# Kernel tuning notes

Measured on AMD Instinct MI355X. Metric: run time of the kernel, lower is better.

Reference implementation:

```python
import jax, jax.numpy as jnp
import numpy as np

TOPK = 13
ALPHA = 1.0
BETA = 6.0
EPS = 1e-9


def _make_boxes(key, lead_shape, img=640.0):
    kc, ks = jax.random.split(key)
    c = jax.random.uniform(kc, lead_shape + (2,), minval=0.0, maxval=img)
    s = jax.random.uniform(ks, lead_shape + (2,), minval=16.0, maxval=160.0)
    return jnp.concatenate([c - s * 0.5, c + s * 0.5], axis=-1)


def setup_inputs() -> dict:
    key = jax.random.key(0)
    ks = jax.random.split(key, 8)
    B, L, C, N, K = 32, 8400, 1, 64, 17
    pred_scores = jax.random.uniform(ks[0], (B, L, C), dtype=jnp.float32)
    pred_bboxes = _make_boxes(ks[1], (B, L))
    pred_poses = jax.random.normal(ks[2], (B, L, K, 3), dtype=jnp.float32)
    anchor_points = jax.random.uniform(ks[3], (L, 2), minval=0.0, maxval=640.0)
    gt_labels = jax.random.randint(ks[4], (B, N, 1), 0, C)
    gt_bboxes = _make_boxes(ks[5], (B, N))
    gt_poses = jax.random.normal(ks[6], (B, N, K, 3), dtype=jnp.float32)
    counts = jax.random.randint(ks[7], (B,), 8, N + 1)
    pad_gt_mask = (jnp.arange(N)[None, :] < counts[:, None]).astype(jnp.float32)[..., None]
    return dict(pred_scores=pred_scores, pred_bboxes=pred_bboxes, pred_poses=pred_poses,
                anchor_points=anchor_points, gt_labels=gt_labels, gt_bboxes=gt_bboxes,
                gt_poses=gt_poses, pad_gt_mask=pad_gt_mask, bg_index=C)


def _batch_iou(box1, box2, eps=EPS):
    # box1: [B,n,4], box2: [B,L,4] -> [B,n,L]
    a = box1[:, :, None, :]
    b = box2[:, None, :, :]
    lt = jnp.maximum(a[..., :2], b[..., :2])
    rb = jnp.minimum(a[..., 2:], b[..., 2:])
    wh = jnp.clip(rb - lt, 0.0)
    inter = wh[..., 0] * wh[..., 1]
    area_a = (a[..., 2] - a[..., 0]) * (a[..., 3] - a[..., 1])
    area_b = (b[..., 2] - b[..., 0]) * (b[..., 3] - b[..., 1])
    return inter / (area_a + area_b - inter + eps)


def _points_in_boxes(points, bboxes, eps=EPS):
    # points: [L,2], bboxes: [B,n,4] -> [B,n,L] float
    x, y = points[:, 0], points[:, 1]
    x1 = bboxes[..., 0:1]; y1 = bboxes[..., 1:2]
    x2 = bboxes[..., 2:3]; y2 = bboxes[..., 3:4]
    m = jnp.minimum(jnp.minimum(x - x1, y - y1), jnp.minimum(x2 - x, y2 - y))
    return (m > eps).astype(bboxes.dtype)


def _gather_topk_anchors(metrics, topk, topk_mask):
    # metrics: [B,n,L]; topk_mask: [B,n,1]
    B, n, L = metrics.shape
    _, idxs = jax.lax.top_k(metrics, topk)  # [B,n,K]
    is_in_topk = jnp.zeros_like(metrics).at[
        jnp.arange(B)[:, None, None], jnp.arange(n)[None, :, None], idxs].add(1.0)
    return is_in_topk * topk_mask


def _compute_max_iou_anchor(ious):
    # ious: [B,n,L] -> one-hot over gt dim of argmax gt per anchor
    n = ious.shape[-2]
    idx = jnp.argmax(ious, axis=-2)  # [B,L]
    return (jnp.arange(n)[None, :, None] == idx[:, None, :]).astype(ious.dtype)


def reference(pred_scores, pred_bboxes, pred_poses, anchor_points, gt_labels,
              gt_bboxes, gt_poses, pad_gt_mask, bg_index):
    B, L, C = pred_scores.shape
    n = gt_bboxes.shape[1]
    K = pred_poses.shape[2]

    ious = _batch_iou(gt_bboxes, pred_bboxes)  # [B,n,L]
    scores_t = jnp.transpose(pred_scores, (0, 2, 1))  # [B,C,L]
    bbox_cls_scores = scores_t[jnp.arange(B)[:, None], gt_labels[..., 0]]  # [B,n,L]
    alignment_metrics = (bbox_cls_scores ** ALPHA) * (ious ** BETA)

    is_in_gts = _points_in_boxes(anchor_points, gt_bboxes)  # [B,n,L]
    is_in_topk = _gather_topk_anchors(alignment_metrics * is_in_gts, TOPK, pad_gt_mask)
    mask_positive = is_in_topk * is_in_gts * pad_gt_mask  # [B,n,L]
    mask_positive_sum = mask_positive.sum(axis=-2)  # [B,L]

    # resolve anchors assigned to multiple gts by max IoU (no-op when no conflicts)
    mask_multiple_gts = jnp.broadcast_to((mask_positive_sum[:, None, :] > 1), mask_positive.shape)
    is_max_iou = _compute_max_iou_anchor(ious)
    mask_positive = jnp.where(mask_multiple_gts, is_max_iou, mask_positive)
    mask_positive_sum = mask_positive.sum(axis=-2)

    assigned_gt_index = jnp.argmax(mask_positive, axis=-2)  # [B,L]
    assigned_gt_index = assigned_gt_index + jnp.arange(B)[:, None] * n  # flat offset
    flat = assigned_gt_index.reshape(-1)

    assigned_labels = jnp.take(gt_labels.reshape(-1), flat).reshape(B, L)
    assigned_labels = jnp.where(mask_positive_sum > 0, assigned_labels,
                                jnp.full_like(assigned_labels, bg_index))
    assigned_bboxes = gt_bboxes.reshape(-1, 4)[flat].reshape(B, L, 4)
    assigned_poses = gt_poses.reshape(-1, K, 3)[flat].reshape(B, L, K, 3)

    one_hot = jax.nn.one_hot(assigned_labels, C + 1, dtype=pred_scores.dtype)
    keep = np.array([i for i in range(C + 1) if i != bg_index])
    assigned_scores = one_hot[..., keep]  # [B,L,C]

    am = alignment_metrics * mask_positive
    max_metrics = am.max(axis=-1, keepdims=True)  # [B,n,1]
    max_ious = (ious * mask_positive).max(axis=-1, keepdims=True)
    am = am / (max_metrics + EPS) * max_ious
    am = am.max(axis=-2)[..., None]  # [B,L,1]
    assigned_scores = assigned_scores * am

    return assigned_labels, assigned_bboxes, assigned_poses, assigned_scores, assigned_gt_index
```

## Files before the change

kernel.cpp:

```cpp
#include <hip/hip_runtime.h>
#include <hip/hip_bf16.h>

#define BB    32
#define LL    8400
#define NGT   64
#define CCH   1
#define KPT   17
#define NTOPK 13
#define POOL  2048
#define NBIN  32

#define OFF_LAB  ((size_t)0)
#define OFF_BOX  ((size_t)268800)
#define OFF_POSE ((size_t)1344000)
#define OFF_SC   ((size_t)15052800)
#define OFF_GI   ((size_t)15321600)


__device__ __forceinline__ float iou_pair(float gx1, float gy1, float gx2, float gy2,
                                          float px1, float py1, float px2, float py2)
{
#pragma clang fp contract(off)
    float ltx = fmaxf(gx1, px1);
    float lty = fmaxf(gy1, py1);
    float rbx = fminf(gx2, px2);
    float rby = fminf(gy2, py2);
    float w = fmaxf(rbx - ltx, 0.0f);
    float h = fmaxf(rby - lty, 0.0f);
    float inter = w * h;
    float ag = (gx2 - gx1) * (gy2 - gy1);
    float ap = (px2 - px1) * (py2 - py1);
    return inter / (ag + ap - inter + 1e-9f);
}

__device__ __forceinline__ bool in_box(float ax, float ay,
                                       float gx1, float gy1, float gx2, float gy2)
{
#pragma clang fp contract(off)
    float m = fminf(fminf(ax - gx1, ay - gy1), fminf(gx2 - ax, gy2 - ay));
    return m > 1e-9f;
}

__device__ __forceinline__ float pow6(float x)
{
#pragma clang fp contract(off)
    float x2 = x * x;
    return (x2 * x2) * x2;
}

__device__ __forceinline__ int bin_of(float x)
{
    int v = (int)floorf(x * 0.05f);
    return v < 0 ? 0 : (v > NBIN - 1 ? NBIN - 1 : v);
}


__global__ __launch_bounds__(256) void clear_kernel(float4* __restrict__ p, int n4)
{
    int t = blockIdx.x * 256 + threadIdx.x;
    if (t < n4) p[t] = make_float4(0.f, 0.f, 0.f, 0.f);
}


__global__ __launch_bounds__(1024) void build_bins_kernel(
    const float* __restrict__ anchor_points,
    int*   __restrict__ bin_start,
    int*   __restrict__ bin_id,
    float2* __restrict__ bin_xy)
{
    __shared__ int c[NBIN * NBIN];
    __shared__ int off[NBIN * NBIN];
    int tid = threadIdx.x;

    c[tid] = 0;
    __syncthreads();
    for (int l = tid; l < LL; l += 1024) {
        float2 ap = reinterpret_cast<const float2*>(anchor_points)[l];
        int bin = bin_of(ap.y) * NBIN + bin_of(ap.x);
        atomicAdd(&c[bin], 1);
    }
    __syncthreads();

    off[tid] = c[tid];
    __syncthreads();
    for (int s = 1; s < NBIN * NBIN; s <<= 1) {
        int v = (tid >= s) ? off[tid - s] : 0;
        __syncthreads();
        off[tid] += v;
        __syncthreads();
    }
    bin_start[tid + 1] = off[tid];
    if (tid == 0) bin_start[0] = 0;
    c[tid] = 0;
    __syncthreads();

    for (int l = tid; l < LL; l += 1024) {
        float2 ap = reinterpret_cast<const float2*>(anchor_points)[l];
        int bin = bin_of(ap.y) * NBIN + bin_of(ap.x);
        int st = (bin == 0) ? 0 : off[bin - 1];
        int slot = st + atomicAdd(&c[bin], 1);
        bin_id[slot] = l;
        bin_xy[slot] = ap;
    }
}


__global__ __launch_bounds__(256) void topk_kernel(
    const float* __restrict__ pred_scores,
    const float* __restrict__ pred_bboxes,
    const float* __restrict__ anchor_points,
    const int*   __restrict__ gt_labels,
    const float* __restrict__ gt_bboxes,
    const float* __restrict__ pad_gt_mask,
    const int*   __restrict__ bin_start,
    const int*   __restrict__ bin_id,
    const float2* __restrict__ bin_xy,
    unsigned*    __restrict__ cells)
{
    __shared__ unsigned long long pool[POOL];
    __shared__ unsigned long long wlists[4 * NTOPK];
    __shared__ int cnt;

    int b = blockIdx.x >> 6;
    int i = blockIdx.x & 63;
    if (pad_gt_mask[b * NGT + i] == 0.0f) return;

    int tid = threadIdx.x;
    if (tid == 0) cnt = 0;
    __syncthreads();

    int gbase = (b * NGT + i) * 4;
    float gx1 = gt_bboxes[gbase + 0];
    float gy1 = gt_bboxes[gbase + 1];
    float gx2 = gt_bboxes[gbase + 2];
    float gy2 = gt_bboxes[gbase + 3];
    int lbl = gt_labels[b * NGT + i];

    int lane = tid & 63;
    int wave = tid >> 6;

    if (tid < 2 * NTOPK) {
        float2 ap = reinterpret_cast<const float2*>(anchor_points)[tid];
        if (!in_box(ap.x, ap.y, gx1, gy1, gx2, gy2)) {
            int slot = atomicAdd(&cnt, 1);
            pool[slot] = (unsigned long long)(0xFFFFFFFFu - (unsigned)tid);
        }
    }

    int bx0 = bin_of(gx1), bx1 = bin_of(gx2);
    int by0 = bin_of(gy1), by1 = bin_of(gy2);
    for (int by = by0; by <= by1; ++by) {
        int s = bin_start[by * NBIN + bx0];
        int e = bin_start[by * NBIN + bx1 + 1];
        for (int t = s + tid; t < e; t += 256) {
            float2 ap = bin_xy[t];
            if (in_box(ap.x, ap.y, gx1, gy1, gx2, gy2)) {
                int l = bin_id[t];
                int pidx = b * LL + l;
                float4 pb = reinterpret_cast<const float4*>(pred_bboxes)[pidx];
                float iou = iou_pair(gx1, gy1, gx2, gy2, pb.x, pb.y, pb.z, pb.w);
                float score = pred_scores[pidx * CCH + lbl];
                float v = score * pow6(iou);
                int slot = atomicAdd(&cnt, 1);
                if (slot < POOL) {
                    pool[slot] =
                        ((unsigned long long)__float_as_uint(v) << 32) |
                        (unsigned long long)(0xFFFFFFFFu - (unsigned)l);
                }
            }
        }
    }
    __syncthreads();

    int total = cnt;
    if (total <= POOL) {
#pragma unroll
        for (int k = 0; k < NTOPK; ++k) {
            unsigned long long lm = 0;
            int li = -1;
            for (int e = wave * 64 + lane; e < total; e += 256) {
                unsigned long long pv = pool[e];
                if (pv > lm) { lm = pv; li = e; }
            }
            unsigned long long m = lm;
#pragma unroll
            for (int off = 32; off > 0; off >>= 1) {
                unsigned long long o = __shfl_xor(m, off);
                m = o > m ? o : m;
            }
            if (lane == 0) wlists[wave * NTOPK + k] = m;
            if (li >= 0 && lm == m) pool[li] = 0;
        }
    } else {
        unsigned long long prev = ~0ull;
        for (int k = 0; k < NTOPK; ++k) {
            unsigned long long lm = 0;
            for (int l = wave * 64 + lane; l < LL; l += 256) {
                int pidx = b * LL + l;
                float4 pb = reinterpret_cast<const float4*>(pred_bboxes)[pidx];
                float iou = iou_pair(gx1, gy1, gx2, gy2, pb.x, pb.y, pb.z, pb.w);
                float score = pred_scores[pidx * CCH + lbl];
                float metric = score * pow6(iou);
                float2 ap = reinterpret_cast<const float2*>(anchor_points)[l];
                float v = in_box(ap.x, ap.y, gx1, gy1, gx2, gy2) ? metric : 0.0f;
                unsigned long long key =
                    ((unsigned long long)__float_as_uint(v) << 32) |
                    (unsigned long long)(0xFFFFFFFFu - (unsigned)l);
                if (key < prev && key > lm) lm = key;
            }
            unsigned long long m = lm;
#pragma unroll
            for (int off = 32; off > 0; off >>= 1) {
                unsigned long long o = __shfl_xor(m, off);
                m = o > m ? o : m;
            }
            if (lane == 0) wlists[wave * NTOPK + k] = m;
            prev = m;
        }
    }
    __syncthreads();

    if (tid == 0) {
        int p0 = 0, p1 = 0, p2 = 0, p3 = 0;
        for (int k = 0; k < NTOPK; ++k) {
            unsigned long long k0 = wlists[0 * NTOPK + p0];
            unsigned long long k1 = wlists[1 * NTOPK + p1];
            unsigned long long k2 = wlists[2 * NTOPK + p2];
            unsigned long long k3 = wlists[3 * NTOPK + p3];
            unsigned long long m01 = k0 >= k1 ? k0 : k1;
            unsigned long long m23 = k2 >= k3 ? k2 : k3;
            unsigned long long m = m01 >= m23 ? m01 : m23;
            if (m == k0)      ++p0;
            else if (m == k1) ++p1;
            else if (m == k2) ++p2;
            else              ++p3;
            if (m == 0ull) continue;

            unsigned lw = 0xFFFFFFFFu - (unsigned)(m & 0xFFFFFFFFull);
            float v = __uint_as_float((unsigned)(m >> 32));
            bool posw;
            if (v > 0.0f) {
                posw = true;
            } else {
                float2 ap = reinterpret_cast<const float2*>(anchor_points)[lw];
                posw = in_box(ap.x, ap.y, gx1, gy1, gx2, gy2);
            }
            if (posw)
                atomicAdd(&cells[b * LL + lw], 1u + ((unsigned)i << 8));
        }
    }
}


__global__ __launch_bounds__(256) void decode_kernel(
    const float* __restrict__ pred_scores,
    const float* __restrict__ pred_bboxes,
    const int*   __restrict__ gt_labels,
    const float* __restrict__ gt_bboxes,
    const unsigned* __restrict__ cells,
    int*      __restrict__ assigned,
    unsigned* __restrict__ rowmax_metric,
    unsigned* __restrict__ rowmax_iou)
{
    __shared__ float gsh[NGT * 4];
    int b = blockIdx.y;
    int tid = threadIdx.x;
    for (int k = tid; k < NGT * 4; k += 256) gsh[k] = gt_bboxes[b * NGT * 4 + k];
    __syncthreads();

    int l = blockIdx.x * 256 + tid;
    if (l >= LL) return;
    int idx = b * LL + l;

    unsigned cell = cells[idx];
    int cnt = (int)(cell & 0xFFu);
    if (cnt == 0) { assigned[idx] = -1; return; }

    float px1 = pred_bboxes[idx * 4 + 0];
    float py1 = pred_bboxes[idx * 4 + 1];
    float px2 = pred_bboxes[idx * 4 + 2];
    float py2 = pred_bboxes[idx * 4 + 3];

    int istar;
    if (cnt == 1) {
        int v = (int)(cell >> 8);
        istar = (v >= 0 && v < NGT) ? v : 0;
    } else {
        float best = -1.0f;
        int bi = 0;
        for (int i = 0; i < NGT; ++i) {
            float iou = iou_pair(gsh[i * 4 + 0], gsh[i * 4 + 1], gsh[i * 4 + 2], gsh[i * 4 + 3],
                                 px1, py1, px2, py2);
            if (iou > best) { best = iou; bi = i; }
        }
        istar = bi;
    }
    assigned[idx] = istar;

    float iou = iou_pair(gsh[istar * 4 + 0], gsh[istar * 4 + 1], gsh[istar * 4 + 2], gsh[istar * 4 + 3],
                         px1, py1, px2, py2);
    int lbl = gt_labels[b * NGT + istar];
    float score = pred_scores[idx * CCH + lbl];
    float met = score * pow6(iou);
    atomicMax(&rowmax_metric[b * NGT + istar], __float_as_uint(met));
    atomicMax(&rowmax_iou[b * NGT + istar], __float_as_uint(iou));
}


__global__ __launch_bounds__(256) void write_kernel(
    const float* __restrict__ pred_scores,
    const float* __restrict__ pred_bboxes,
    const int*   __restrict__ gt_labels,
    const float* __restrict__ gt_bboxes,
    const int*      __restrict__ assigned,
    const unsigned* __restrict__ rowmax_metric,
    const unsigned* __restrict__ rowmax_iou,
    const int*   __restrict__ bg_ptr,
    float* __restrict__ out)
{
    __shared__ float gsh[NGT * 4];
    int b = blockIdx.y;
    int tid = threadIdx.x;
    for (int k = tid; k < NGT * 4; k += 256) gsh[k] = gt_bboxes[b * NGT * 4 + k];
    __syncthreads();

    int l = blockIdx.x * 256 + tid;
    if (l >= LL) return;
    int idx = b * LL + l;

    int a = assigned[idx];
    bool pos = a >= 0;
    int agi = pos ? a : 0;
    int bg = *bg_ptr;
    int lbl = pos ? gt_labels[b * NGT + agi] : bg;

    out[OFF_LAB + (size_t)idx] = (float)lbl;
    out[OFF_GI + (size_t)idx]  = (float)(b * NGT + agi);

    float4 box;
    box.x = gsh[agi * 4 + 0];
    box.y = gsh[agi * 4 + 1];
    box.z = gsh[agi * 4 + 2];
    box.w = gsh[agi * 4 + 3];
    reinterpret_cast<float4*>(out + OFF_BOX)[idx] = box;

    float am = 0.0f;
    if (pos) {
        float px1 = pred_bboxes[idx * 4 + 0];
        float py1 = pred_bboxes[idx * 4 + 1];
        float px2 = pred_bboxes[idx * 4 + 2];
        float py2 = pred_bboxes[idx * 4 + 3];
        float iou = iou_pair(box.x, box.y, box.z, box.w, px1, py1, px2, py2);
        float score = pred_scores[idx * CCH + gt_labels[b * NGT + a]];
        float met = score * pow6(iou);
        float mm = __uint_as_float(rowmax_metric[b * NGT + a]);
        float mi = __uint_as_float(rowmax_iou[b * NGT + a]);
        am = met / (mm + 1e-9f) * mi;
    }
    int kc = (bg == 0) ? 1 : 0;
    out[OFF_SC + (size_t)idx] = (lbl == kc) ? am : 0.0f;
}


__global__ __launch_bounds__(256) void pose_kernel(
    const float* __restrict__ gt_poses,
    const int*   __restrict__ assigned,
    float* __restrict__ out_poses)
{
    const int TOT4 = BB * LL * KPT * 3 / 4;
    int c = blockIdx.x * 256 + threadIdx.x;
    if (c >= TOT4) return;
    int e0 = c * 4;
    float r[4];
#pragma unroll
    for (int u = 0; u < 4; ++u) {
        int e = e0 + u;
        int anchor = e / (KPT * 3);
        int j = e - anchor * (KPT * 3);
        int b = anchor / LL;
        int a = assigned[anchor];
        int agi = a >= 0 ? a : 0;
        r[u] = gt_poses[(size_t)(b * NGT + agi) * (KPT * 3) + j];
    }
    float4 v;
    v.x = r[0]; v.y = r[1]; v.z = r[2]; v.w = r[3];
    reinterpret_cast<float4*>(out_poses)[c] = v;
}


extern "C" void kernel_launch(void* const* d_in, const int* in_sizes, int n_in,
                              void* d_out, int out_size, void* d_ws, size_t ws_size,
                              hipStream_t stream)
{
    const float* pred_scores   = (const float*)d_in[0];
    const float* pred_bboxes   = (const float*)d_in[1];
    const float* anchor_points = (const float*)d_in[3];
    const int*   gt_labels     = (const int*)d_in[4];
    const float* gt_bboxes     = (const float*)d_in[5];
    const float* gt_poses      = (const float*)d_in[6];
    const float* pad_gt_mask   = (const float*)d_in[7];
    const int*   bg_ptr        = (const int*)d_in[8];

    char* ws = (char*)d_ws;
    unsigned* cells         = (unsigned*)ws;
    unsigned* rowmax_metric = (unsigned*)(ws + 1075200);
    unsigned* rowmax_iou    = (unsigned*)(ws + 1083392);
    int*      assigned      = (int*)(ws + 1091584);
    int*      bin_start     = (int*)(ws + 2166784);
    int*      bin_id        = (int*)(ws + 2170888);
    float2*   bin_xy        = (float2*)(ws + 2204488);

    const int N4 = 1091584 / 16;
    clear_kernel<<<(N4 + 255) / 256, 256, 0, stream>>>((float4*)d_ws, N4);

    build_bins_kernel<<<1, 1024, 0, stream>>>(anchor_points, bin_start, bin_id, bin_xy);

    topk_kernel<<<BB * NGT, 256, 0, stream>>>(
        pred_scores, pred_bboxes, anchor_points, gt_labels, gt_bboxes, pad_gt_mask,
        bin_start, bin_id, bin_xy, cells);

    dim3 gridBL((LL + 255) / 256, BB);
    decode_kernel<<<gridBL, 256, 0, stream>>>(
        pred_scores, pred_bboxes, gt_labels, gt_bboxes, cells,
        assigned, rowmax_metric, rowmax_iou);

    write_kernel<<<gridBL, 256, 0, stream>>>(
        pred_scores, pred_bboxes, gt_labels, gt_bboxes,
        assigned, rowmax_metric, rowmax_iou, bg_ptr, (float*)d_out);

    const int TOT4 = BB * LL * KPT * 3 / 4;
    pose_kernel<<<(TOT4 + 255) / 256, 256, 0, stream>>>(
        gt_poses, assigned, (float*)d_out + OFF_POSE);
}
```

Baseline: 95.66 us.

## Parallelize anchor binning across blocks and shrink topk to one wave per GT

The single-block anchor binning kernel is split into three kernels: a parallel count with global atomics, a single-block scan, and a parallel scatter. The topk kernel now runs one 64-thread wave per GT, which drops the per-wave candidate lists and the serial 4-way merge on thread 0. Each of the first 13 lanes keeps one winner and issues its own atomic. The pool shrinks to 1024 entries to lower LDS use and raise occupancy. The risks are more frequent fallback to the full-scan path for large boxes, extra launch overhead, and less parallelism within each GT.

After: 88.64 us, median of 2. -7.3%, faster.

```diff
diff --git a/kernel.cpp b/kernel.cpp
--- a/kernel.cpp
+++ b/kernel.cpp
@@ -7,7 +7,7 @@
 #define CCH   1
 #define KPT   17
 #define NTOPK 13
-#define POOL  2048
+#define POOL  1024
 #define NBIN  32
 
 #define OFF_LAB  ((size_t)0)
@@ -15,6 +15,16 @@
 #define OFF_POSE ((size_t)1344000)
 #define OFF_SC   ((size_t)15052800)
 #define OFF_GI   ((size_t)15321600)
+
+#define WS_CELLS    0
+#define WS_RM       1075200
+#define WS_RI       1083392
+#define WS_ASSIGNED 1091584
+#define WS_BINCNT   2166784
+#define WS_BINSTART 2170880
+#define WS_BINCUR   2174984
+#define WS_BINID    2179080
+#define WS_BINXY    2212680
 
 
 __device__ __forceinline__ float iou_pair(float gx1, float gy1, float gx2, float gy2,
@@ -55,33 +65,34 @@
 }
 
 
-__global__ __launch_bounds__(256) void clear_kernel(float4* __restrict__ p, int n4)
-{
+__global__ __launch_bounds__(256) void clear_kernel(char* __restrict__ ws)
+{
+    const int N4A = 1091584 / 16;
+    const int N4B = 4096 / 16;
     int t = blockIdx.x * 256 + threadIdx.x;
-    if (t < n4) p[t] = make_float4(0.f, 0.f, 0.f, 0.f);
-}
-
-
-__global__ __launch_bounds__(1024) void build_bins_kernel(
-    const float* __restrict__ anchor_points,
-    int*   __restrict__ bin_start,
-    int*   __restrict__ bin_id,
-    float2* __restrict__ bin_xy)
-{
-    __shared__ int c[NBIN * NBIN];
+    if (t < N4A)
+        reinterpret_cast<float4*>(ws + WS_CELLS)[t] = make_float4(0.f, 0.f, 0.f, 0.f);
+    else if (t < N4A + N4B)
+        reinterpret_cast<float4*>(ws + WS_BINCNT)[t - N4A] = make_float4(0.f, 0.f, 0.f, 0.f);
+}
+
+
+__global__ __launch_bounds__(256) void count_kernel(
+    const float* __restrict__ anchor_points, int* __restrict__ bin_cnt)
+{
+    int l = blockIdx.x * 256 + threadIdx.x;
+    if (l >= LL) return;
+    float2 ap = reinterpret_cast<const float2*>(anchor_points)[l];
+    atomicAdd(&bin_cnt[bin_of(ap.y) * NBIN + bin_of(ap.x)], 1);
+}
+
+__global__ __launch_bounds__(1024) void scan_kernel(
+    const int* __restrict__ bin_cnt,
+    int* __restrict__ bin_start, int* __restrict__ bin_cursor)
+{
     __shared__ int off[NBIN * NBIN];
     int tid = threadIdx.x;
-
-    c[tid] = 0;
-    __syncthreads();
-    for (int l = tid; l < LL; l += 1024) {
-        float2 ap = reinterpret_cast<const float2*>(anchor_points)[l];
-        int bin = bin_of(ap.y) * NBIN + bin_of(ap.x);
-        atomicAdd(&c[bin], 1);
-    }
-    __syncthreads();
-
-    off[tid] = c[tid];
+    off[tid] = bin_cnt[tid];
     __syncthreads();
     for (int s = 1; s < NBIN * NBIN; s <<= 1) {
         int v = (tid >= s) ? off[tid - s] : 0;
@@ -90,22 +101,27 @@
         __syncthreads();
     }
     bin_start[tid + 1] = off[tid];
+    int excl = (tid == 0) ? 0 : off[tid - 1];
+    bin_cursor[tid] = excl;
     if (tid == 0) bin_start[0] = 0;
-    c[tid] = 0;
-    __syncthreads();
-
-    for (int l = tid; l < LL; l += 1024) {
-        float2 ap = reinterpret_cast<const float2*>(anchor_points)[l];
-        int bin = bin_of(ap.y) * NBIN + bin_of(ap.x);
-        int st = (bin == 0) ? 0 : off[bin - 1];
-        int slot = st + atomicAdd(&c[bin], 1);
-        bin_id[slot] = l;
-        bin_xy[slot] = ap;
-    }
-}
-
-
-__global__ __launch_bounds__(256) void topk_kernel(
+}
+
+__global__ __launch_bounds__(256) void scatter_kernel(
+    const float* __restrict__ anchor_points,
+    int* __restrict__ bin_cursor,
+    int* __restrict__ bin_id, float2* __restrict__ bin_xy)
+{
+    int l = blockIdx.x * 256 + threadIdx.x;
+    if (l >= LL) return;
+    float2 ap = reinterpret_cast<const float2*>(anchor_points)[l];
+    int bin = bin_of(ap.y) * NBIN + bin_of(ap.x);
+    int slot = atomicAdd(&bin_cursor[bin], 1);
+    bin_id[slot] = l;
+    bin_xy[slot] = ap;
+}
+
+
+__global__ __launch_bounds__(64) void topk_kernel(
     const float* __restrict__ pred_scores,
     const float* __restrict__ pred_bboxes,
     const float* __restrict__ anchor_points,
@@ -118,15 +134,14 @@
     unsigned*    __restrict__ cells)
 {
     __shared__ unsigned long long pool[POOL];
-    __shared__ unsigned long long wlists[4 * NTOPK];
     __shared__ int cnt;
 
     int b = blockIdx.x >> 6;
     int i = blockIdx.x & 63;
     if (pad_gt_mask[b * NGT + i] == 0.0f) return;
 
-    int tid = threadIdx.x;
-    if (tid == 0) cnt = 0;
+    int lane = threadIdx.x;
+    if (lane == 0) cnt = 0;
     __syncthreads();
 
     int gbase = (b * NGT + i) * 4;
@@ -136,14 +151,11 @@
     float gy2 = gt_bboxes[gbase + 3];
     int lbl = gt_labels[b * NGT + i];
 
-    int lane = tid & 63;
-    int wave = tid >> 6;
-
-    if (tid < 2 * NTOPK) {
-        float2 ap = reinterpret_cast<const float2*>(anchor_points)[tid];
+    if (lane < 2 * NTOPK) {
+        float2 ap = reinterpret_cast<const float2*>(anchor_points)[lane];
         if (!in_box(ap.x, ap.y, gx1, gy1, gx2, gy2)) {
             int slot = atomicAdd(&cnt, 1);
-            pool[slot] = (unsigned long long)(0xFFFFFFFFu - (unsigned)tid);
+            pool[slot] = (unsigned long long)(0xFFFFFFFFu - (unsigned)lane);
         }
     }
 
@@ -152,7 +164,7 @@
     for (int by = by0; by <= by1; ++by) {
         int s = bin_start[by * NBIN + bx0];
         int e = bin_start[by * NBIN + bx1 + 1];
-        for (int t = s + tid; t < e; t += 256) {
+        for (int t = s + lane; t < e; t += 64) {
             float2 ap = bin_xy[t];
             if (in_box(ap.x, ap.y, gx1, gy1, gx2, gy2)) {
                 int l = bin_id[t];
@@ -173,12 +185,13 @@
     __syncthreads();
 
     int total = cnt;
+    unsigned long long winner = 0;
     if (total <= POOL) {
 #pragma unroll
         for (int k = 0; k < NTOPK; ++k) {
             unsigned long long lm = 0;
             int li = -1;
-            for (int e = wave * 64 + lane; e < total; e += 256) {
+            for (int e = lane; e < total; e += 64) {
                 unsigned long long pv = pool[e];
                 if (pv > lm) { lm = pv; li = e; }
             }
@@ -188,14 +201,15 @@
                 unsigned long long o = __shfl_xor(m, off);
                 m = o > m ? o : m;
             }
-            if (lane == 0) wlists[wave * NTOPK + k] = m;
+            if (lane == k) winner = m;
             if (li >= 0 && lm == m) pool[li] = 0;
         }
     } else {
         unsigned long long prev = ~0ull;
+#pragma unroll 1
         for (int k = 0; k < NTOPK; ++k) {
             unsigned long long lm = 0;
-            for (int l = wave * 64 + lane; l < LL; l += 256) {
+            for (int l = lane; l < LL; l += 64) {
                 int pidx = b * LL + l;
                 float4 pb = reinterpret_cast<const float4*>(pred_bboxes)[pidx];
                 float iou = iou_pair(gx1, gy1, gx2, gy2, pb.x, pb.y, pb.z, pb.w);
@@ -214,40 +228,23 @@
                 unsigned long long o = __shfl_xor(m, off);
                 m = o > m ? o : m;
             }
-            if (lane == 0) wlists[wave * NTOPK + k] = m;
+            if (lane == k) winner = m;
             prev = m;
         }
     }
-    __syncthreads();
-
-    if (tid == 0) {
-        int p0 = 0, p1 = 0, p2 = 0, p3 = 0;
-        for (int k = 0; k < NTOPK; ++k) {
-            unsigned long long k0 = wlists[0 * NTOPK + p0];
-            unsigned long long k1 = wlists[1 * NTOPK + p1];
-            unsigned long long k2 = wlists[2 * NTOPK + p2];
-            unsigned long long k3 = wlists[3 * NTOPK + p3];
-            unsigned long long m01 = k0 >= k1 ? k0 : k1;
-            unsigned long long m23 = k2 >= k3 ? k2 : k3;
-            unsigned long long m = m01 >= m23 ? m01 : m23;
-            if (m == k0)      ++p0;
-            else if (m == k1) ++p1;
-            else if (m == k2) ++p2;
-            else              ++p3;
-            if (m == 0ull) continue;
-
-            unsigned lw = 0xFFFFFFFFu - (unsigned)(m & 0xFFFFFFFFull);
-            float v = __uint_as_float((unsigned)(m >> 32));
-            bool posw;
-            if (v > 0.0f) {
-                posw = true;
-            } else {
-                float2 ap = reinterpret_cast<const float2*>(anchor_points)[lw];
-                posw = in_box(ap.x, ap.y, gx1, gy1, gx2, gy2);
-            }
-            if (posw)
-                atomicAdd(&cells[b * LL + lw], 1u + ((unsigned)i << 8));
-        }
+
+    if (lane < NTOPK && winner != 0ull) {
+        unsigned lw = 0xFFFFFFFFu - (unsigned)(winner & 0xFFFFFFFFull);
+        float v = __uint_as_float((unsigned)(winner >> 32));
+        bool posw;
+        if (v > 0.0f) {
+            posw = true;
+        } else {
+            float2 ap = reinterpret_cast<const float2*>(anchor_points)[lw];
+            posw = in_box(ap.x, ap.y, gx1, gy1, gx2, gy2);
+        }
+        if (posw)
+            atomicAdd(&cells[b * LL + lw], 1u + ((unsigned)i << 8));
     }
 }
 
@@ -402,20 +399,25 @@
     const int*   bg_ptr        = (const int*)d_in[8];
 
     char* ws = (char*)d_ws;
-    unsigned* cells         = (unsigned*)ws;
-    unsigned* rowmax_metric = (unsigned*)(ws + 1075200);
-    unsigned* rowmax_iou    = (unsigned*)(ws + 1083392);
-    int*      assigned      = (int*)(ws + 1091584);
-    int*      bin_start     = (int*)(ws + 2166784);
-    int*      bin_id        = (int*)(ws + 2170888);
-    float2*   bin_xy        = (float2*)(ws + 2204488);
-
-    const int N4 = 1091584 / 16;
-    clear_kernel<<<(N4 + 255) / 256, 256, 0, stream>>>((float4*)d_ws, N4);
-
-    build_bins_kernel<<<1, 1024, 0, stream>>>(anchor_points, bin_start, bin_id, bin_xy);
-
-    topk_kernel<<<BB * NGT, 256, 0, stream>>>(
+    unsigned* cells         = (unsigned*)(ws + WS_CELLS);
+    unsigned* rowmax_metric = (unsigned*)(ws + WS_RM);
+    unsigned* rowmax_iou    = (unsigned*)(ws + WS_RI);
+    int*      assigned      = (int*)(ws + WS_ASSIGNED);
+    int*      bin_cnt       = (int*)(ws + WS_BINCNT);
+    int*      bin_start     = (int*)(ws + WS_BINSTART);
+    int*      bin_cursor    = (int*)(ws + WS_BINCUR);
+    int*      bin_id        = (int*)(ws + WS_BINID);
+    float2*   bin_xy        = (float2*)(ws + WS_BINXY);
+
+    const int NCLR = (1091584 + 4096) / 16;
+    clear_kernel<<<(NCLR + 255) / 256, 256, 0, stream>>>(ws);
+
+    int ablocks = (LL + 255) / 256;
+    count_kernel<<<ablocks, 256, 0, stream>>>(anchor_points, bin_cnt);
+    scan_kernel<<<1, 1024, 0, stream>>>(bin_cnt, bin_start, bin_cursor);
+    scatter_kernel<<<ablocks, 256, 0, stream>>>(anchor_points, bin_cursor, bin_id, bin_xy);
+
+    topk_kernel<<<BB * NGT, 64, 0, stream>>>(
         pred_scores, pred_bboxes, anchor_points, gt_labels, gt_bboxes, pad_gt_mask,
         bin_start, bin_id, bin_xy, cells);
 
```
